# Kernel tuning notes

Measured on AMD Instinct MI355X. Metric: run time of the kernel, lower is better.

## Reference

```python
import jax, jax.numpy as jnp
import numpy as np

N, D_IN, H, E = 8192, 2048, 1024, 8

def setup_inputs() -> dict:
    key = jax.random.key(0)
    ks = jax.random.split(key, 12)
    s = lambda k, shp, fan: jax.random.normal(k, shp, jnp.float32) * (1.0 / np.sqrt(fan))
    return {
        "x": jax.random.normal(ks[0], (N, D_IN), jnp.float32),
        "enc_W": s(ks[1], (D_IN, H), D_IN),
        "enc_b": jnp.zeros((H,), jnp.float32),
        "gate_W": s(ks[2], (H, E), H),
        "expert_W": s(ks[3], (E, H, H), H),
        "expert_b": jnp.zeros((E, H), jnp.float32),
        "mlp_W": s(ks[4], (H, H), H),
        "mlp_b": jnp.zeros((H,), jnp.float32),
        "coef_W": s(ks[5], (H, 2), H),
        "coef_b": jnp.zeros((2,), jnp.float32),
        "dec_W": s(ks[6], (H, D_IN), H),
        "dec_b": jnp.zeros((D_IN,), jnp.float32),
    }

def reference(x, enc_W, enc_b, gate_W, expert_W, expert_b,
              mlp_W, mlp_b, coef_W, coef_b, dec_W, dec_b):
    # encoder + relu
    h = jax.nn.relu(x @ enc_W + enc_b)                       # [N,H]
    # top-1 gate
    probs = jax.nn.softmax(h @ gate_W, axis=-1)              # [N,E]
    idx = jnp.argmax(probs, axis=-1)                         # [N]
    p = jnp.take_along_axis(probs, idx[:, None], axis=1)     # [N,1]
    onehot = jax.nn.one_hot(idx, probs.shape[-1], dtype=h.dtype)  # [N,E]
    # dispatch -> per-expert GEMM -> combine
    xe = jnp.einsum('ne,nh->enh', onehot, h)                 # [E,N,H]
    ye = jnp.einsum('enh,ehd->end', xe, expert_W) + expert_b[:, None, :]
    moe_out = jnp.einsum('ne,end->nd', onehot, ye) * p       # [N,H]
    # residual MoE mixing
    mlp_out = h @ mlp_W + mlp_b                              # [N,H]
    coef = jax.nn.softmax(h @ coef_W + coef_b, axis=-1)      # [N,2]
    out = moe_out * coef[:, 0:1] + mlp_out * coef[:, 1:2]
    # decoder
    return out @ dec_W + dec_b                               # [N,D_IN]
```

## Files before the change

kernel.cpp:

```cpp
#include <hip/hip_runtime.h>
#include <hip/hip_bf16.h>
#include <stdint.h>


using bf16 = __hip_bfloat16;
typedef __bf16 bf16x8 __attribute__((ext_vector_type(8)));
typedef float f32x4 __attribute__((ext_vector_type(4)));

static constexpr int NROWS = 8192;
static constexpr int DIN   = 2048;
static constexpr int HD    = 1024;
static constexpr int NEXP  = 8;
static constexpr int MAX_TILES = 72;
static constexpr int MAXFLAG  = 512;
static constexpr int MAXFLAG2 = 128;
static constexpr int F1Z = 7;
#define GAPTHR  0.02f
#define GAPTHR2 1.0e-3

__device__ __forceinline__ uint16_t f2u(float f) {
  bf16 h = __float2bfloat16(f);
  uint16_t u; __builtin_memcpy(&u, &h, 2); return u;
}
__device__ __forceinline__ float u2f(uint16_t u) {
  uint32_t x = ((uint32_t)u) << 16;
  float f; __builtin_memcpy(&f, &x, 4); return f;
}

typedef const __attribute__((address_space(1))) void* gas_ptr;
typedef __attribute__((address_space(3))) void* las_ptr;
__device__ __forceinline__ void async16(void* lds, const void* g) {
  __builtin_amdgcn_global_load_lds((gas_ptr)g, (las_ptr)lds, 16, 0, 0);
}

__global__ __launch_bounds__(256)
void prep_kernel(const float* __restrict__ x, uint16_t* __restrict__ x_bf,
                 const float* __restrict__ encW, uint16_t* __restrict__ encWT,
                 const float* __restrict__ mlpW, uint16_t* __restrict__ mlpWT,
                 const float* __restrict__ decW, uint16_t* __restrict__ decWT,
                 const float* __restrict__ expW, uint16_t* __restrict__ expWT,
                 int* __restrict__ ctrs_i)
{
  __shared__ float tile[64 * 65];
  const int b = blockIdx.x;
  const int t = threadIdx.x;
  if (b == 0 && t < 64) ctrs_i[t] = 0;

  if (b < 1024) {
    for (int i = b * 256 + t; i < NROWS * DIN / 8; i += 1024 * 256) {
      const float* s = x + (size_t)i * 8;
      float4 v0 = *(const float4*)(s);
      float4 v1 = *(const float4*)(s + 4);
      uint16_t tmp[8];
      tmp[0]=f2u(v0.x); tmp[1]=f2u(v0.y); tmp[2]=f2u(v0.z); tmp[3]=f2u(v0.w);
      tmp[4]=f2u(v1.x); tmp[5]=f2u(v1.y); tmp[6]=f2u(v1.z); tmp[7]=f2u(v1.w);
      int4 pv; __builtin_memcpy(&pv, tmp, 16);
      *(int4*)(x_bf + (size_t)i * 8) = pv;
    }
    return;
  }
  const float* in; uint16_t* out; int R, C, bx, by;
  int q = b - 1024;
  if (q < 512)       { in = encW; out = encWT; R = DIN; C = HD;  bx = q & 15; by = q >> 4; }
  else if (q < 768)  { q -= 512;  in = mlpW; out = mlpWT; R = HD; C = HD;  bx = q & 15; by = q >> 4; }
  else if (q < 1280) { q -= 768;  in = decW; out = decWT; R = HD; C = DIN; bx = q & 31; by = q >> 5; }
  else { q -= 1280; const int z = q >> 8; q &= 255;
         in = expW + (size_t)z * HD * HD; out = expWT + (size_t)z * HD * HD;
         R = HD; C = HD; bx = q & 15; by = q >> 4; }
  const int C0 = bx * 64, R0 = by * 64;
  const int cl = (t & 7) * 8;
#pragma unroll
  for (int p = 0; p < 2; ++p) {
    const int r = p * 32 + (t >> 3);
    const float* src = in + (size_t)(R0 + r) * C + C0 + cl;
    float4 v0 = *(const float4*)(src);
    float4 v1 = *(const float4*)(src + 4);
    float* dst = &tile[r * 65 + cl];
    dst[0]=v0.x; dst[1]=v0.y; dst[2]=v0.z; dst[3]=v0.w;
    dst[4]=v1.x; dst[5]=v1.y; dst[6]=v1.z; dst[7]=v1.w;
  }
  __syncthreads();
#pragma unroll
  for (int p = 0; p < 2; ++p) {
    const int oc = p * 32 + (t >> 3);
    uint16_t tmp[8];
#pragma unroll
    for (int j = 0; j < 8; ++j) tmp[j] = f2u(tile[(cl + j) * 65 + oc]);
    int4 v; __builtin_memcpy(&v, tmp, 16);
    *(int4*)(out + (size_t)(C0 + oc) * R + R0 + cl) = v;
  }
}

template<int MODE>
__device__ __forceinline__
void gemm_body(const uint16_t* __restrict__ A, const uint16_t* __restrict__ BT,
               uint16_t* __restrict__ C16, float* __restrict__ C32,
               const float* __restrict__ biasf,
               const int* __restrict__ rowperm, const int* __restrict__ tinfo,
               const float* __restrict__ scale, int M, int N, int K)
{
  __shared__ uint16_t As[2][128 * 64];
  __shared__ uint16_t Bs[2][128 * 64];

  const int t = threadIdx.x;
  const int nty = gridDim.y;
  const int nwg = gridDim.x * nty;
  const int hwf = blockIdx.y * gridDim.x + blockIdx.x;
  const int swz = (hwf & 7) * (nwg >> 3) + (hwf >> 3);
  const int mtile = swz / nty;
  const int ntile = swz % nty;

  int e = 0, row0 = 0, rowend = 0;
  if constexpr (MODE == 1) {
    const int nt = tinfo[0];
    if (mtile >= nt) return;
    e      = tinfo[1 + mtile * 3 + 0];
    row0   = tinfo[1 + mtile * 3 + 1];
    rowend = tinfo[1 + mtile * 3 + 2];
  }

  const int kcol = (t & 7) * 8;
  const uint16_t* asrc[4];
  const uint16_t* bsrc[4];
#pragma unroll
  for (int c = 0; c < 4; ++c) {
    const int r = c * 32 + (t >> 3);
    int arow;
    if constexpr (MODE == 1) {
      int pr = row0 + r;
      if (pr > rowend - 1) pr = rowend - 1;
      arow = rowperm[pr];
    } else {
      arow = mtile * 128 + r;
    }
    asrc[c] = A + (size_t)arow * K + kcol;
    size_t brow = (size_t)ntile * 128 + r;
    if constexpr (MODE == 1) brow += (size_t)e * N;
    bsrc[c] = BT + brow * (size_t)K + kcol;
  }

  f32x4 acc[4][4];
  const f32x4 zero = {0.f, 0.f, 0.f, 0.f};
#pragma unroll
  for (int i = 0; i < 4; ++i)
#pragma unroll
    for (int j = 0; j < 4; ++j) acc[i][j] = zero;

  const int wid = t >> 6, lane = t & 63;
  const int wm = wid >> 1, wn = wid & 1;
  const int frow = lane & 15;
  const int fk = (lane >> 4) * 8;

  const int nk = K >> 6;
#pragma unroll
  for (int c = 0; c < 4; ++c) {
    async16(&As[0][c * 2048 + t * 8], asrc[c]);
    async16(&Bs[0][c * 2048 + t * 8], bsrc[c]);
  }
  __syncthreads();

  int cur = 0;
  for (int kt = 0; kt < nk; ++kt) {
    if (kt + 1 < nk) {
#pragma unroll
      for (int c = 0; c < 4; ++c) {
        async16(&As[cur ^ 1][c * 2048 + t * 8], asrc[c] + (kt + 1) * 64);
        async16(&Bs[cur ^ 1][c * 2048 + t * 8], bsrc[c] + (kt + 1) * 64);
      }
    }
#pragma unroll
    for (int kk = 0; kk < 2; ++kk) {
      bf16x8 af[4], bfr[4];
#pragma unroll
      for (int mi = 0; mi < 4; ++mi)
        af[mi] = *reinterpret_cast<const bf16x8*>(
            &As[cur][(wm * 64 + mi * 16 + frow) * 64 + kk * 32 + fk]);
#pragma unroll
      for (int ni = 0; ni < 4; ++ni)
        bfr[ni] = *reinterpret_cast<const bf16x8*>(
            &Bs[cur][(wn * 64 + ni * 16 + frow) * 64 + kk * 32 + fk]);
#pragma unroll
      for (int mi = 0; mi < 4; ++mi)
#pragma unroll
        for (int ni = 0; ni < 4; ++ni)
          acc[mi][ni] = __builtin_amdgcn_mfma_f32_16x16x32_bf16(
              af[mi], bfr[ni], acc[mi][ni], 0, 0, 0);
    }
    __syncthreads();
    cur ^= 1;
  }

  const int nbase = ntile * 128 + wn * 64;
  const int rbase = wm * 64 + (lane >> 4) * 4;
  const int cbase = lane & 15;
#pragma unroll
  for (int mi = 0; mi < 4; ++mi) {
#pragma unroll
    for (int j = 0; j < 4; ++j) {
      const int rr = rbase + mi * 16 + j;
      if constexpr (MODE == 1) {
        const int pr = row0 + rr;
        if (pr < rowend) {
          const int orig = rowperm[pr];
          const float sc = scale[orig];
          uint16_t* dst = C16 + (size_t)orig * N;
#pragma unroll
          for (int ni = 0; ni < 4; ++ni) {
            const int gc = nbase + ni * 16 + cbase;
            dst[gc] = f2u((acc[mi][ni][j] + biasf[e * N + gc]) * sc);
          }
        }
      } else {
        const int gr = mtile * 128 + rr;
#pragma unroll
        for (int ni = 0; ni < 4; ++ni) {
          const int gc = nbase + ni * 16 + cbase;
          float v = acc[mi][ni][j] + biasf[gc];
          if constexpr (MODE == 0) {
            C16[(size_t)gr * N + gc] = f2u(fmaxf(v, 0.f));
          } else if constexpr (MODE == 2) {
            const float prev = u2f(C16[(size_t)gr * N + gc]);
            C16[(size_t)gr * N + gc] = f2u(prev + v * scale[gr]);
          } else {
            C32[(size_t)gr * N + gc] = v;
          }
        }
      }
    }
  }
}

__global__ __launch_bounds__(256)
void gemm_enc(const uint16_t* A, const uint16_t* BT, uint16_t* C16,
              const float* biasf, int M, int N, int K) {
  gemm_body<0>(A, BT, C16, nullptr, biasf, nullptr, nullptr, nullptr, M, N, K);
}
__global__ __launch_bounds__(256)
void gemm_moe(const uint16_t* A, const uint16_t* BT, uint16_t* C16,
              const float* biasf, const int* rowperm, const int* tinfo,
              const float* scale, int M, int N, int K) {
  gemm_body<1>(A, BT, C16, nullptr, biasf, rowperm, tinfo, scale, M, N, K);
}
__global__ __launch_bounds__(256)
void gemm_mlp(const uint16_t* A, const uint16_t* BT, uint16_t* C16,
              const float* biasf, const float* scale, int M, int N, int K) {
  gemm_body<2>(A, BT, C16, nullptr, biasf, nullptr, nullptr, scale, M, N, K);
}
__global__ __launch_bounds__(256)
void gemm_dec(const uint16_t* A, const uint16_t* BT, float* C32,
              const float* biasf, int M, int N, int K) {
  gemm_body<3>(A, BT, nullptr, C32, biasf, nullptr, nullptr, nullptr, M, N, K);
}

__global__ __launch_bounds__(256)
void gate_kernel(const uint16_t* __restrict__ hbf, const float* __restrict__ gW,
                 const float* __restrict__ cW, const float* __restrict__ cb,
                 int* __restrict__ eidx, float* __restrict__ s0,
                 float* __restrict__ c1, int* __restrict__ nflag,
                 int* __restrict__ flaglist)
{
  const int lane = threadIdx.x & 63;
  const int row  = blockIdx.x * 4 + (threadIdx.x >> 6);
  const uint16_t* hrow = hbf + (size_t)row * HD;
  float a[10];
#pragma unroll
  for (int i = 0; i < 10; ++i) a[i] = 0.f;
  for (int kk = 0; kk < HD / 64; ++kk) {
    const int k = kk * 64 + lane;
    const float hv = u2f(hrow[k]);
    float4 g0 = *(const float4*)(gW + (size_t)k * 8);
    float4 g1 = *(const float4*)(gW + (size_t)k * 8 + 4);
    a[0] += hv * g0.x; a[1] += hv * g0.y; a[2] += hv * g0.z; a[3] += hv * g0.w;
    a[4] += hv * g1.x; a[5] += hv * g1.y; a[6] += hv * g1.z; a[7] += hv * g1.w;
    float2 cv = *(const float2*)(cW + (size_t)k * 2);
    a[8] += hv * cv.x; a[9] += hv * cv.y;
  }
#pragma unroll
  for (int off = 32; off > 0; off >>= 1) {
#pragma unroll
    for (int i = 0; i < 10; ++i) a[i] += __shfl_xor(a[i], off);
  }
  if (lane == 0) {
    int best = 0; float bm = a[0];
#pragma unroll
    for (int e2 = 1; e2 < 8; ++e2) if (a[e2] > bm) { bm = a[e2]; best = e2; }
    float sec = -3.0e38f;
#pragma unroll
    for (int e2 = 0; e2 < 8; ++e2) if (e2 != best) sec = fmaxf(sec, a[e2]);
    float s = 0.f;
#pragma unroll
    for (int e2 = 0; e2 < 8; ++e2) s += expf(a[e2] - bm);
    const float p  = 1.f / s;
    const float l0 = a[8] + cb[0], l1 = a[9] + cb[1];
    const float mx = fmaxf(l0, l1);
    const float e0 = expf(l0 - mx), e1 = expf(l1 - mx);
    const float inv = 1.f / (e0 + e1);
    eidx[row] = best;
    s0[row]   = p * (e0 * inv);
    c1[row]   = e1 * inv;
    if (bm - sec < GAPTHR) {
      int fi = atomicAdd(nflag, 1);
      if (fi < MAXFLAG) flaglist[fi] = row;
    }
  }
}

template<typename T>
__global__ __launch_bounds__(256)
void fixup1_kernel(const float* __restrict__ x, const float* __restrict__ encW,
                   const int* __restrict__ flaglist, const int* __restrict__ nflag,
                   T* __restrict__ zpart, int fstride, int maxflag)
{
  __shared__ float xs[8][128];
  __shared__ T red[8][4][64];
  int nf = *nflag; if (nf > maxflag) nf = maxflag;
  if (nf <= 0) return;
  const int rs = blockIdx.z;
  const int nb = (nf + 7) >> 3;
  if (rs >= nb) return;
  const int t  = threadIdx.x;
  const int jb = blockIdx.x, kb = blockIdx.y;
  const int tj = t & 63, tk = t >> 6;
  const int j  = jb * 64 + tj;
  const int k0 = kb * 128 + tk * 32;
  float w[32];
#pragma unroll
  for (int kk = 0; kk < 32; ++kk)
    w[kk] = encW[(size_t)(k0 + kk) * HD + j];

  for (int fb = rs; fb < nb; fb += F1Z) {
    __syncthreads();
    {
      const int r  = t >> 5;
      const int kc = (t & 31) * 4;
      int f = fb * 8 + r; if (f > nf - 1) f = nf - 1;
      const int row = flaglist[f];
      *(float4*)&xs[r][kc] =
          *(const float4*)&x[(size_t)row * DIN + kb * 128 + kc];
    }
    __syncthreads();
    T acc[8];
#pragma unroll
    for (int r = 0; r < 8; ++r) acc[r] = (T)0;
#pragma unroll
    for (int kq = 0; kq < 8; ++kq) {
      float4 xv[8];
#pragma unroll
      for (int r = 0; r < 8; ++r)
        xv[r] = *(const float4*)&xs[r][tk * 32 + kq * 4];
#pragma unroll
      for (int r = 0; r < 8; ++r) {
        acc[r] += (T)xv[r].x * (T)w[kq * 4 + 0];
        acc[r] += (T)xv[r].y * (T)w[kq * 4 + 1];
        acc[r] += (T)xv[r].z * (T)w[kq * 4 + 2];
        acc[r] += (T)xv[r].w * (T)w[kq * 4 + 3];
      }
    }
#pragma unroll
    for (int r = 0; r < 8; ++r) red[r][tk][tj] = acc[r];
    __syncthreads();
#pragma unroll
    for (int p = 0; p < 2; ++p) {
      const int idx = p * 256 + t;
      const int r = idx >> 6, jj = idx & 63;
      const int f = fb * 8 + r;
      if (f < nf)
        zpart[((size_t)kb * fstride + f) * HD + jb * 64 + jj] =
            (red[r][0][jj] + red[r][1][jj]) + (red[r][2][jj] + red[r][3][jj]);
    }
  }
}

template<int STAGE, typename T>
__global__ __launch_bounds__(256)
void fixup2_kernel(const T* __restrict__ zpart, const float* __restrict__ encB,
                   const float* __restrict__ gW, const float* __restrict__ cW,
                   const float* __restrict__ cb, const int* __restrict__ flaglist,
                   const int* __restrict__ nflag, int* __restrict__ eidx,
                   float* __restrict__ s0, float* __restrict__ c1,
                   int* __restrict__ nflag2, int* __restrict__ flaglist2,
                   int fstride, int maxflag)
{
  __shared__ double red[4][10];
  int nf = *nflag; if (nf > maxflag) nf = maxflag;
  const int t = threadIdx.x, lane = t & 63, w = t >> 6;
  for (int f = blockIdx.x; f < nf; f += 128) {
    const int row = flaglist[f];
    double part[10];
#pragma unroll
    for (int i = 0; i < 10; ++i) part[i] = 0.0;
    for (int jj = t; jj < HD; jj += 256) {
      double z = 0.0;
#pragma unroll
      for (int kb = 0; kb < 16; ++kb)
        z += (double)zpart[((size_t)kb * fstride + f) * HD + jj];
      double hj = z + (double)encB[jj];
      hj = hj > 0.0 ? hj : 0.0;
      const float* gr = gW + (size_t)jj * 8;
#pragma unroll
      for (int e2 = 0; e2 < 8; ++e2) part[e2] += hj * (double)gr[e2];
      part[8] += hj * (double)cW[jj * 2];
      part[9] += hj * (double)cW[jj * 2 + 1];
    }
#pragma unroll
    for (int off = 32; off > 0; off >>= 1)
#pragma unroll
      for (int i = 0; i < 10; ++i) part[i] += __shfl_xor(part[i], off);
    if (lane == 0)
#pragma unroll
      for (int i = 0; i < 10; ++i) red[w][i] = part[i];
    __syncthreads();
    if (t == 0) {
      double a[10];
#pragma unroll
      for (int i = 0; i < 10; ++i)
        a[i] = red[0][i] + red[1][i] + red[2][i] + red[3][i];
      int best = 0; double bm = a[0];
#pragma unroll
      for (int e2 = 1; e2 < 8; ++e2) if (a[e2] > bm) { bm = a[e2]; best = e2; }
      double sec = -1.0e300;
#pragma unroll
      for (int e2 = 0; e2 < 8; ++e2) if (e2 != best && a[e2] > sec) sec = a[e2];
      double s = 0.0;
#pragma unroll
      for (int e2 = 0; e2 < 8; ++e2) s += exp(a[e2] - bm);
      const double p  = 1.0 / s;
      const double l0 = a[8] + (double)cb[0], l1 = a[9] + (double)cb[1];
      const double mx = l0 > l1 ? l0 : l1;
      const double e0 = exp(l0 - mx), e1 = exp(l1 - mx);
      const double inv = 1.0 / (e0 + e1);
      eidx[row] = best;
      s0[row]   = (float)(p * e0 * inv);
      c1[row]   = (float)(e1 * inv);
      if constexpr (STAGE == 0) {
        if (bm - sec < GAPTHR2) {
          int fi = atomicAdd(nflag2, 1);
          if (fi < MAXFLAG2) flaglist2[fi] = row;
        }
      }
    }
    __syncthreads();
  }
}

__global__ __launch_bounds__(1024)
void scan_scatter_kernel(const int* __restrict__ eidx,
                         int* __restrict__ tinfo, int* __restrict__ rowperm)
{
  __shared__ int scnt[NEXP];
  __shared__ int soffs[NEXP];
  __shared__ int scur[NEXP];
  const int t = threadIdx.x;
  if (t < NEXP) scnt[t] = 0;
  __syncthreads();
  for (int n = t; n < NROWS; n += 1024)
    atomicAdd(&scnt[eidx[n]], 1);
  __syncthreads();
  if (t == 0) {
    int off = 0, nt = 0;
    for (int e = 0; e < NEXP; ++e) {
      soffs[e] = off; scur[e] = 0;
      const int c = scnt[e];
      const int end = off + c;
      for (int r = 0; r < c; r += 128) {
        tinfo[1 + nt * 3 + 0] = e;
        tinfo[1 + nt * 3 + 1] = off + r;
        tinfo[1 + nt * 3 + 2] = end;
        ++nt;
      }
      off = end;
    }
    tinfo[0] = nt;
  }
  __syncthreads();
  for (int n = t; n < NROWS; n += 1024) {
    const int e = eidx[n];
    rowperm[soffs[e] + atomicAdd(&scur[e], 1)] = n;
  }
}

extern "C" void kernel_launch(void* const* d_in, const int* in_sizes, int n_in,
                              void* d_out, int out_size, void* d_ws, size_t ws_size,
                              hipStream_t stream) {
  (void)in_sizes; (void)n_in; (void)out_size;
  const float* x      = (const float*)d_in[0];
  const float* enc_W  = (const float*)d_in[1];
  const float* enc_b  = (const float*)d_in[2];
  const float* gate_W = (const float*)d_in[3];
  const float* exp_W  = (const float*)d_in[4];
  const float* exp_b  = (const float*)d_in[5];
  const float* mlp_W  = (const float*)d_in[6];
  const float* mlp_b  = (const float*)d_in[7];
  const float* coef_W = (const float*)d_in[8];
  const float* coef_b = (const float*)d_in[9];
  const float* dec_W  = (const float*)d_in[10];
  const float* dec_b  = (const float*)d_in[11];

  char* ws = (char*)d_ws;
  size_t off = 0;
  auto alloc = [&](size_t bytes) {
    char* p = ws + off;
    off += (bytes + 255) & ~(size_t)255;
    return p;
  };
  uint16_t* encWT  = (uint16_t*)alloc((size_t)DIN * HD * 2);
  uint16_t* mlpWT  = (uint16_t*)alloc((size_t)HD * HD * 2);
  uint16_t* decWT  = (uint16_t*)alloc((size_t)HD * DIN * 2);
  uint16_t* expWT  = (uint16_t*)alloc((size_t)NEXP * HD * HD * 2);
  uint16_t* h_bf   = (uint16_t*)alloc((size_t)NROWS * HD * 2);
  float*    zpart  = (float*)   alloc((size_t)16 * MAXFLAG * HD * 4);
  int*      eidx   = (int*)     alloc(NROWS * 4);
  float*    s0     = (float*)   alloc(NROWS * 4);
  float*    c1     = (float*)   alloc(NROWS * 4);
  int*      rowperm= (int*)     alloc(NROWS * 4);
  int*      flags  = (int*)     alloc(MAXFLAG * 4);
  int*      flags2 = (int*)     alloc(MAXFLAG2 * 4);
  char*     ctrs   = (char*)    alloc(256);
  int*      tinfo  = (int*)     alloc((1 + MAX_TILES * 3) * 4 + 64);
  uint16_t* x_bf   = (uint16_t*)zpart;
  double*   zpartB = (double*)zpart;
  uint16_t* accout = (uint16_t*)zpart;
  int*      nflag  = (int*)(ctrs + 32);
  int*      nflag2 = (int*)(ctrs + 64);
  if (off > ws_size) return;

  const dim3 blk(256);
  prep_kernel<<<dim3(4352), blk, 0, stream>>>(
      x, x_bf, enc_W, encWT, mlp_W, mlpWT, dec_W, decWT, exp_W, expWT,
      (int*)ctrs);

  gemm_enc<<<dim3(NROWS / 128, HD / 128), blk, 0, stream>>>(
      x_bf, encWT, h_bf, enc_b, NROWS, HD, DIN);

  gate_kernel<<<dim3(NROWS / 4), blk, 0, stream>>>(
      h_bf, gate_W, coef_W, coef_b, eidx, s0, c1, nflag, flags);

  fixup1_kernel<float><<<dim3(16, 16, F1Z), blk, 0, stream>>>(
      x, enc_W, flags, nflag, zpart, MAXFLAG, MAXFLAG);
  fixup2_kernel<0, float><<<dim3(128), blk, 0, stream>>>(
      zpart, enc_b, gate_W, coef_W, coef_b, flags, nflag, eidx, s0, c1,
      nflag2, flags2, MAXFLAG, MAXFLAG);
  fixup1_kernel<double><<<dim3(16, 16, F1Z), blk, 0, stream>>>(
      x, enc_W, flags2, nflag2, zpartB, MAXFLAG2, MAXFLAG2);
  fixup2_kernel<1, double><<<dim3(128), blk, 0, stream>>>(
      zpartB, enc_b, gate_W, coef_W, coef_b, flags2, nflag2, eidx, s0, c1,
      nullptr, nullptr, MAXFLAG2, MAXFLAG2);

  scan_scatter_kernel<<<dim3(1), dim3(1024), 0, stream>>>(
      eidx, tinfo, rowperm);

  gemm_moe<<<dim3(MAX_TILES, HD / 128), blk, 0, stream>>>(
      h_bf, expWT, accout, exp_b, rowperm, tinfo, s0, NROWS, HD, HD);
  gemm_mlp<<<dim3(NROWS / 128, HD / 128), blk, 0, stream>>>(
      h_bf, mlpWT, accout, mlp_b, c1, NROWS, HD, HD);
  gemm_dec<<<dim3(NROWS / 128, DIN / 128), blk, 0, stream>>>(
      accout, decWT, (float*)d_out, dec_b, NROWS, DIN, HD);
}
```

Baseline: 316.9 us.

## Use 256x128 tile, 8-wave GEMM with swizzled LDS for dense layers

Adds a new GEMM body for the encoder, MLP and decoder GEMMs. It uses 256x128 tiles with 512 threads (8 waves) and XOR-swizzled LDS addresses to avoid bank conflicts. Loads are double-buffered with a vmcnt-based wait, and MFMA sections are raised to higher s_setprio. The MoE GEMM keeps the old 128x128 path as a standalone kernel. The larger tiles are meant to raise arithmetic intensity and cut LDS conflicts, at the cost of more LDS and registers per block and fewer blocks in the grid.

```diff
diff --git a/kernel.cpp b/kernel.cpp
--- a/kernel.cpp
+++ b/kernel.cpp
@@ -93,11 +93,143 @@
 
 template<int MODE>
 __device__ __forceinline__
-void gemm_body(const uint16_t* __restrict__ A, const uint16_t* __restrict__ BT,
-               uint16_t* __restrict__ C16, float* __restrict__ C32,
-               const float* __restrict__ biasf,
-               const int* __restrict__ rowperm, const int* __restrict__ tinfo,
-               const float* __restrict__ scale, int M, int N, int K)
+void gemm8p_body(const uint16_t* __restrict__ A, const uint16_t* __restrict__ BT,
+                 uint16_t* __restrict__ C16, float* __restrict__ C32,
+                 const float* __restrict__ biasf, const float* __restrict__ scale,
+                 int M, int N, int K)
+{
+  constexpr int BM = 256, BN = 128, BK = 64;
+  __shared__ uint16_t As[2][BM * BK];
+  __shared__ uint16_t Bs[2][BN * BK];
+
+  const int t = threadIdx.x;
+  const int ntyg = gridDim.y;
+  const int nwg  = gridDim.x * ntyg;
+  const int hwf  = blockIdx.y * gridDim.x + blockIdx.x;
+  const int swzb = (hwf & 7) * (nwg >> 3) + (hwf >> 3);
+  const int mtile = swzb / ntyg;
+  const int ntile = swzb % ntyg;
+
+  const int trow = t >> 3;
+  const int cbD  = (t & 7) * 16;
+  const int cbS  = cbD ^ ((trow & 7) << 4);
+  const char* aRow[4];
+  const char* bRow[2];
+#pragma unroll
+  for (int c = 0; c < 4; ++c)
+    aRow[c] = (const char*)A + ((size_t)(mtile * BM + c * 64 + trow) * K) * 2 + cbS;
+#pragma unroll
+  for (int c = 0; c < 2; ++c)
+    bRow[c] = (const char*)BT + ((size_t)(ntile * BN + c * 64 + trow) * K) * 2 + cbS;
+
+  auto stage = [&](int b, int kt) {
+#pragma unroll
+    for (int c = 0; c < 4; ++c)
+      async16(&As[b][c * 4096 + t * 8], aRow[c] + (size_t)kt * 128);
+#pragma unroll
+    for (int c = 0; c < 2; ++c)
+      async16(&Bs[b][c * 4096 + t * 8], bRow[c] + (size_t)kt * 128);
+  };
+
+  const int wid = t >> 6, lane = t & 63;
+  const int wm = wid >> 2, wn = wid & 3;
+  const int frow = lane & 15, hi = lane >> 4;
+
+  f32x4 acc[8][2];
+  const f32x4 zero = {0.f, 0.f, 0.f, 0.f};
+#pragma unroll
+  for (int i = 0; i < 8; ++i) { acc[i][0] = zero; acc[i][1] = zero; }
+
+  auto ldfrag = [&](const uint16_t* base, int row, int kk) {
+    const int cb = (kk * 64 + hi * 16) ^ ((row & 7) << 4);
+    return *reinterpret_cast<const bf16x8*>(
+        reinterpret_cast<const char*>(base) + row * 128 + cb);
+  };
+
+  const int nt = K >> 6;
+  stage(0, 0);
+  stage(1, 1);
+
+  for (int kt = 0; kt < nt; ++kt) {
+    const int b = kt & 1;
+    asm volatile("s_waitcnt vmcnt(6)" ::: "memory");
+    __builtin_amdgcn_s_barrier();
+
+    bf16x8 af[8][2], bfr[2][2];
+#pragma unroll
+    for (int mi = 0; mi < 8; ++mi)
+#pragma unroll
+      for (int kk = 0; kk < 2; ++kk)
+        af[mi][kk] = ldfrag(As[b], wm * 128 + mi * 16 + frow, kk);
+#pragma unroll
+    for (int ni = 0; ni < 2; ++ni)
+#pragma unroll
+      for (int kk = 0; kk < 2; ++kk)
+        bfr[ni][kk] = ldfrag(Bs[b], wn * 32 + ni * 16 + frow, kk);
+
+    asm volatile("s_waitcnt lgkmcnt(0)" ::: "memory");
+    __builtin_amdgcn_s_barrier();
+
+    if (kt + 2 < nt) stage(b, kt + 2);
+
+    __builtin_amdgcn_s_setprio(1);
+#pragma unroll
+    for (int kk = 0; kk < 2; ++kk)
+#pragma unroll
+      for (int mi = 0; mi < 8; ++mi)
+#pragma unroll
+        for (int ni = 0; ni < 2; ++ni)
+          acc[mi][ni] = __builtin_amdgcn_mfma_f32_16x16x32_bf16(
+              af[mi][kk], bfr[ni][kk], acc[mi][ni], 0, 0, 0);
+    __builtin_amdgcn_s_setprio(0);
+  }
+
+  const int nbase = ntile * BN + wn * 32;
+  const int rbase = mtile * BM + wm * 128 + hi * 4;
+  const int cbase = lane & 15;
+#pragma unroll
+  for (int mi = 0; mi < 8; ++mi) {
+#pragma unroll
+    for (int j = 0; j < 4; ++j) {
+      const int gr = rbase + mi * 16 + j;
+#pragma unroll
+      for (int ni = 0; ni < 2; ++ni) {
+        const int gc = nbase + ni * 16 + cbase;
+        float v = acc[mi][ni][j] + biasf[gc];
+        if constexpr (MODE == 0) {
+          C16[(size_t)gr * N + gc] = f2u(fmaxf(v, 0.f));
+        } else if constexpr (MODE == 2) {
+          const float prev = u2f(C16[(size_t)gr * N + gc]);
+          C16[(size_t)gr * N + gc] = f2u(prev + v * scale[gr]);
+        } else {
+          C32[(size_t)gr * N + gc] = v;
+        }
+      }
+    }
+  }
+}
+
+__global__ __launch_bounds__(512)
+void gemm_enc(const uint16_t* A, const uint16_t* BT, uint16_t* C16,
+              const float* biasf, int M, int N, int K) {
+  gemm8p_body<0>(A, BT, C16, nullptr, biasf, nullptr, M, N, K);
+}
+__global__ __launch_bounds__(512)
+void gemm_mlp(const uint16_t* A, const uint16_t* BT, uint16_t* C16,
+              const float* biasf, const float* scale, int M, int N, int K) {
+  gemm8p_body<2>(A, BT, C16, nullptr, biasf, scale, M, N, K);
+}
+__global__ __launch_bounds__(512)
+void gemm_dec(const uint16_t* A, const uint16_t* BT, float* C32,
+              const float* biasf, int M, int N, int K) {
+  gemm8p_body<3>(A, BT, nullptr, C32, biasf, nullptr, M, N, K);
+}
+
+__global__ __launch_bounds__(256)
+void gemm_moe(const uint16_t* __restrict__ A, const uint16_t* __restrict__ BT,
+              uint16_t* __restrict__ C16, const float* __restrict__ biasf,
+              const int* __restrict__ rowperm, const int* __restrict__ tinfo,
+              const float* __restrict__ scale, int M, int N, int K)
 {
   __shared__ uint16_t As[2][128 * 64];
   __shared__ uint16_t Bs[2][128 * 64];
@@ -110,14 +242,11 @@
   const int mtile = swz / nty;
   const int ntile = swz % nty;
 
-  int e = 0, row0 = 0, rowend = 0;
-  if constexpr (MODE == 1) {
-    const int nt = tinfo[0];
-    if (mtile >= nt) return;
-    e      = tinfo[1 + mtile * 3 + 0];
-    row0   = tinfo[1 + mtile * 3 + 1];
-    rowend = tinfo[1 + mtile * 3 + 2];
-  }
+  const int nt2 = tinfo[0];
+  if (mtile >= nt2) return;
+  const int e      = tinfo[1 + mtile * 3 + 0];
+  const int row0   = tinfo[1 + mtile * 3 + 1];
+  const int rowend = tinfo[1 + mtile * 3 + 2];
 
   const int kcol = (t & 7) * 8;
   const uint16_t* asrc[4];
@@ -125,18 +254,10 @@
 #pragma unroll
   for (int c = 0; c < 4; ++c) {
     const int r = c * 32 + (t >> 3);
-    int arow;
-    if constexpr (MODE == 1) {
-      int pr = row0 + r;
-      if (pr > rowend - 1) pr = rowend - 1;
-      arow = rowperm[pr];
-    } else {
-      arow = mtile * 128 + r;
-    }
-    asrc[c] = A + (size_t)arow * K + kcol;
-    size_t brow = (size_t)ntile * 128 + r;
-    if constexpr (MODE == 1) brow += (size_t)e * N;
-    bsrc[c] = BT + brow * (size_t)K + kcol;
+    int pr = row0 + r;
+    if (pr > rowend - 1) pr = rowend - 1;
+    asrc[c] = A + (size_t)rowperm[pr] * K + kcol;
+    bsrc[c] = BT + ((size_t)e * N + ntile * 128 + r) * (size_t)K + kcol;
   }
 
   f32x4 acc[4][4];
@@ -197,59 +318,19 @@
   for (int mi = 0; mi < 4; ++mi) {
 #pragma unroll
     for (int j = 0; j < 4; ++j) {
-      const int rr = rbase + mi * 16 + j;
-      if constexpr (MODE == 1) {
-        const int pr = row0 + rr;
-        if (pr < rowend) {
-          const int orig = rowperm[pr];
-          const float sc = scale[orig];
-          uint16_t* dst = C16 + (size_t)orig * N;
-#pragma unroll
-          for (int ni = 0; ni < 4; ++ni) {
-            const int gc = nbase + ni * 16 + cbase;
-            dst[gc] = f2u((acc[mi][ni][j] + biasf[e * N + gc]) * sc);
-          }
-        }
-      } else {
-        const int gr = mtile * 128 + rr;
+      const int pr = row0 + rbase + mi * 16 + j;
+      if (pr < rowend) {
+        const int orig = rowperm[pr];
+        const float sc = scale[orig];
+        uint16_t* dst = C16 + (size_t)orig * N;
 #pragma unroll
         for (int ni = 0; ni < 4; ++ni) {
           const int gc = nbase + ni * 16 + cbase;
-          float v = acc[mi][ni][j] + biasf[gc];
-          if constexpr (MODE == 0) {
-            C16[(size_t)gr * N + gc] = f2u(fmaxf(v, 0.f));
-          } else if constexpr (MODE == 2) {
-            const float prev = u2f(C16[(size_t)gr * N + gc]);
-            C16[(size_t)gr * N + gc] = f2u(prev + v * scale[gr]);
-          } else {
-            C32[(size_t)gr * N + gc] = v;
-          }
+          dst[gc] = f2u((acc[mi][ni][j] + biasf[e * N + gc]) * sc);
         }
       }
     }
   }
-}
-
-__global__ __launch_bounds__(256)
-void gemm_enc(const uint16_t* A, const uint16_t* BT, uint16_t* C16,
-              const float* biasf, int M, int N, int K) {
-  gemm_body<0>(A, BT, C16, nullptr, biasf, nullptr, nullptr, nullptr, M, N, K);
-}
-__global__ __launch_bounds__(256)
-void gemm_moe(const uint16_t* A, const uint16_t* BT, uint16_t* C16,
-              const float* biasf, const int* rowperm, const int* tinfo,
-              const float* scale, int M, int N, int K) {
-  gemm_body<1>(A, BT, C16, nullptr, biasf, rowperm, tinfo, scale, M, N, K);
-}
-__global__ __launch_bounds__(256)
-void gemm_mlp(const uint16_t* A, const uint16_t* BT, uint16_t* C16,
-              const float* biasf, const float* scale, int M, int N, int K) {
-  gemm_body<2>(A, BT, C16, nullptr, biasf, nullptr, nullptr, scale, M, N, K);
-}
-__global__ __launch_bounds__(256)
-void gemm_dec(const uint16_t* A, const uint16_t* BT, float* C32,
-              const float* biasf, int M, int N, int K) {
-  gemm_body<3>(A, BT, nullptr, C32, biasf, nullptr, nullptr, nullptr, M, N, K);
 }
 
 __global__ __launch_bounds__(256)
@@ -529,7 +610,7 @@
       x, x_bf, enc_W, encWT, mlp_W, mlpWT, dec_W, decWT, exp_W, expWT,
       (int*)ctrs);
 
-  gemm_enc<<<dim3(NROWS / 128, HD / 128), blk, 0, stream>>>(
+  gemm_enc<<<dim3(NROWS / 256, HD / 128), dim3(512), 0, stream>>>(
       x_bf, encWT, h_bf, enc_b, NROWS, HD, DIN);
 
   gate_kernel<<<dim3(NROWS / 4), blk, 0, stream>>>(
@@ -551,8 +632,8 @@
 
   gemm_moe<<<dim3(MAX_TILES, HD / 128), blk, 0, stream>>>(
       h_bf, expWT, accout, exp_b, rowperm, tinfo, s0, NROWS, HD, HD);
-  gemm_mlp<<<dim3(NROWS / 128, HD / 128), blk, 0, stream>>>(
+  gemm_mlp<<<dim3(NROWS / 256, HD / 128), dim3(512), 0, stream>>>(
       h_bf, mlpWT, accout, mlp_b, c1, NROWS, HD, HD);
-  gemm_dec<<<dim3(NROWS / 128, DIN / 128), blk, 0, stream>>>(
+  gemm_dec<<<dim3(NROWS / 256, DIN / 128), dim3(512), 0, stream>>>(
       accout, decWT, (float*)d_out, dec_b, NROWS, DIN, HD);
 }
```

New measurement: 291.7 us. -8.0%, faster.
